# Kernel optimization log

Hardware: AMD Instinct MI355X
Metric: run time of the kernel (lower is better)

## Reference

```python
import jax, jax.numpy as jnp
import numpy as np

B, D_IN = 2048, 16
Q, QD = 512, 2
H = 128

def setup_inputs() -> dict:
    key = jax.random.key(0)
    ks = jax.random.split(key, 7)
    return {
        "input": jax.random.normal(ks[0], (B, D_IN), dtype=jnp.float32),
        "eq_param": jax.random.normal(ks[1], (QD, 1), dtype=jnp.float32),
        "quad_x": jax.random.uniform(ks[2], (Q, QD), dtype=jnp.float32),
        "W1": jax.random.normal(ks[3], (QD + D_IN, H), dtype=jnp.float32) * (1.0 / np.sqrt(QD + D_IN)),
        "b1": jnp.zeros((H,), dtype=jnp.float32),
        "W2": jax.random.normal(ks[4], (H, 1), dtype=jnp.float32) * (1.0 / np.sqrt(H)),
        "b2": jnp.zeros((1,), dtype=jnp.float32),
    }

def reference(input, eq_param, quad_x, W1, b1, W2, b2):
    # input: [B, d_in], quad_x: [Q, qd]
    b, d = input.shape
    q, qd = quad_x.shape
    # x = quad_x.repeat(B,1) -> [B,Q,qd]; z = input repeated per quad row -> [B,Q,d]
    x = jnp.broadcast_to(quad_x[None, :, :], (b, q, qd))
    z = jnp.broadcast_to(input[:, None, :], (b, q, d))
    concat = jnp.concatenate([x, z], axis=-1)            # [B,Q,qd+d]
    h = jnp.tanh(concat @ W1 + b1)                       # [B,Q,H]
    lhs = h @ W2 + b2                                    # [B,Q,1]  (mlp_x)
    y = jnp.sin(x @ eq_param)                            # [B,Q,1]  (r_func)
    rhs = lhs * y
    # per-row segment sum over Q quadrature points (and scalar out dim)
    out = jnp.sum(rhs, axis=(1, 2))[:, None]             # [B,1]
    return out
```

## Files before the change

kernel.cpp:

```cpp
#include <hip/hip_runtime.h>
#include <math.h>

#define B_N   2048
#define D_IN_ 16
#define Q_N   512
#define H_N   128

#define QCHUNK 32
#define NQC    (Q_N / QCHUNK)
#define QPC    (QCHUNK / 4)
#define NB     8
#define RPB    16
#define NRB    (B_N / RPB)

#define COEF_OFF 0
#define K0_OFF   131072
#define F_OFF    131136

static constexpr float kC = 2.88539008177792681472f;

__global__ __launch_bounds__(256) void precompute_kernel(
    const float* __restrict__ input,
    const float* __restrict__ eq,
    const float* __restrict__ qx,
    const float* __restrict__ W1,
    const float* __restrict__ b1,
    const float* __restrict__ W2,
    const float* __restrict__ b2,
    float* __restrict__ ws)
{
    const int blk = blockIdx.x;
    const int t   = threadIdx.x;

    if (blk < 1024) {
        const int idx = blk * 256 + t;
        const int row = idx >> 7, h = idx & 127;
        const float* inr = input + row * D_IN_;
        float s = 0.0f;
        #pragma unroll
        for (int d = 0; d < D_IN_; ++d)
            s = fmaf(inr[d], W1[(2 + d) * H_N + h], s);
        ws[F_OFF + idx] = __builtin_amdgcn_exp2f(s * kC);
    } else if (blk < 1088) {
        const int set  = (blk - 1024) * 256 + t;
        const int quad = set >> 7, h = set & 127;
        const float w1a = W1[h], w1b = W1[H_N + h], bh = b1[h];
        const float e0 = eq[0], e1 = eq[1];
        float n0 = 0, n1 = 0, n2 = 0, n3 = 0;
        float p1 = 0, p2 = 0, p3 = 0, p4 = 0;
        #pragma unroll
        for (int i = 0; i < 4; ++i) {
            const int q = quad * 4 + i;
            const float x0 = qx[2 * q], x1 = qx[2 * q + 1];
            const float u = fmaf(x1, w1b, fmaf(x0, w1a, bh));
            const float E = __builtin_amdgcn_exp2f(u * kC);
            const float y = -2.0f * sinf(fmaf(x1, e1, x0 * e0));
            n3 = fmaf(E, n2, fmaf(y, p3, n3));
            n2 = fmaf(E, n1, fmaf(y, p2, n2));
            n1 = fmaf(E, n0, fmaf(y, p1, n1));
            n0 = n0 + y;
            p4 = fmaf(E, p3, p4);
            p3 = fmaf(E, p2, p3);
            p2 = fmaf(E, p1, p2);
            p1 = p1 + E;
        }
        float* dst = ws + COEF_OFF + quad * (8 * H_N) + h;
        dst[0 * H_N] = n0; dst[1 * H_N] = n1; dst[2 * H_N] = n2; dst[3 * H_N] = n3;
        dst[4 * H_N] = p1; dst[5 * H_N] = p2; dst[6 * H_N] = p3; dst[7 * H_N] = p4;
    } else {
        __shared__ float red[8];
        const float e0 = eq[0], e1 = eq[1];
        const int lane = t & 63, w = t >> 6;
        float s = 0.0f;
        #pragma unroll
        for (int i = 0; i < 2; ++i) {
            const int q = t + 256 * i;
            s += sinf(fmaf(qx[2 * q + 1], e1, qx[2 * q] * e0));
        }
        #pragma unroll
        for (int off = 32; off >= 1; off >>= 1)
            s += __shfl_down(s, off, 64);
        if (lane == 0) red[w] = s;
        float ws2 = (t < H_N) ? W2[t] : 0.0f;
        if (w < 2) {
            #pragma unroll
            for (int off = 32; off >= 1; off >>= 1)
                ws2 += __shfl_down(ws2, off, 64);
            if (lane == 0) red[4 + w] = ws2;
        }
        __syncthreads();
        if (t == 0) {
            const float S = red[0] + red[1] + red[2] + red[3];
            ws[K0_OFF] = S * (red[4] + red[5] + b2[0]);
        }
    }
}

__global__ __launch_bounds__(256, 4) void main_kernel(
    const float* __restrict__ ws,
    const float* __restrict__ W2,
    float* __restrict__ out)
{
    __shared__ float c_s[QPC * 8 * H_N];
    __shared__ float part[4][NB];

    const int t    = threadIdx.x;
    const int rb   = blockIdx.x & (NRB - 1);
    const int qc   = blockIdx.x >> 7;
    const int h    = t & 127;
    const int bg   = t >> 7;
    const int lane = t & 63;
    const int w    = t >> 6;

    {
        const float4* src = (const float4*)(ws + COEF_OFF + qc * (QPC * 8 * H_N));
        float4* dst = (float4*)c_s;
        #pragma unroll
        for (int i = 0; i < (QPC * 8 * H_N / 4) / 256; ++i)
            dst[t + 256 * i] = src[t + 256 * i];
    }

    const int rowBase = rb * RPB + bg * NB;
    float F[NB], acc[NB];
    #pragma unroll
    for (int r = 0; r < NB; ++r) {
        F[r] = ws[F_OFF + (rowBase + r) * H_N + h];
        acc[r] = 0.0f;
    }
    __syncthreads();

    #pragma unroll
    for (int qd = 0; qd < QPC; ++qd) {
        const float* cp = c_s + qd * (8 * H_N) + h;
        const float n0 = cp[0 * H_N], n1 = cp[1 * H_N];
        const float n2 = cp[2 * H_N], n3 = cp[3 * H_N];
        const float c1 = cp[4 * H_N], c2 = cp[5 * H_N];
        const float c3 = cp[6 * H_N], c4 = cp[7 * H_N];
        #pragma unroll
        for (int r = 0; r < NB; ++r) {
            const float Fr  = F[r];
            const float den = fmaf(fmaf(fmaf(fmaf(c4, Fr, c3), Fr, c2), Fr, c1), Fr, 1.0f);
            const float num = fmaf(fmaf(fmaf(n3, Fr, n2), Fr, n1), Fr, n0);
            acc[r] = fmaf(num, __builtin_amdgcn_rcpf(den), acc[r]);
        }
    }

    const float w2 = W2[h];
    #pragma unroll
    for (int r = 0; r < NB; ++r) {
        float p = acc[r] * w2;
        #pragma unroll
        for (int off = 32; off >= 1; off >>= 1)
            p += __shfl_down(p, off, 64);
        if (lane == 0) part[w][r] = p;
    }
    __syncthreads();

    if (t < 16) {
        const int r = t & 7, g = t >> 3;
        float s = part[2 * g][r] + part[2 * g + 1][r];
        if (qc == 0) s += ws[K0_OFF];
        atomicAdd(out + rb * RPB + g * NB + r, s);
    }
}

extern "C" void kernel_launch(void* const* d_in, const int* in_sizes, int n_in,
                              void* d_out, int out_size, void* d_ws, size_t ws_size,
                              hipStream_t stream)
{
    (void)in_sizes; (void)n_in; (void)ws_size;
    const float* input = (const float*)d_in[0];
    const float* eq    = (const float*)d_in[1];
    const float* qx    = (const float*)d_in[2];
    const float* W1    = (const float*)d_in[3];
    const float* b1    = (const float*)d_in[4];
    const float* W2    = (const float*)d_in[5];
    const float* b2    = (const float*)d_in[6];
    float* out = (float*)d_out;
    float* ws  = (float*)d_ws;

    hipMemsetAsync(d_out, 0, (size_t)out_size * sizeof(float), stream);
    precompute_kernel<<<dim3(1089), dim3(256), 0, stream>>>(
        input, eq, qx, W1, b1, W2, b2, ws);
    main_kernel<<<dim3(NRB * NQC), dim3(256), 0, stream>>>(ws, W2, out);
}
```

Before: 83.76 us.

## Fuse precompute into main kernel, recomputing coefficients and features per block

Removes the separate precompute kernel and its global workspace. Each block now computes its own q-chunk rational coefficients, its per-row exp features and a per-chunk constant term in shared memory. This removes one launch, the workspace writes and reads, and the serialization between kernels. In exchange it adds redundant per-block recomputation of coefficients, transcendental calls and extra shared memory.

```diff
diff --git a/kernel.cpp b/kernel.cpp
--- a/kernel.cpp
+++ b/kernel.cpp
@@ -13,13 +13,9 @@
 #define RPB    16
 #define NRB    (B_N / RPB)
 
-#define COEF_OFF 0
-#define K0_OFF   131072
-#define F_OFF    131136
-
 static constexpr float kC = 2.88539008177792681472f;
 
-__global__ __launch_bounds__(256) void precompute_kernel(
+__global__ __launch_bounds__(256, 4) void fused_kernel(
     const float* __restrict__ input,
     const float* __restrict__ eq,
     const float* __restrict__ qx,
@@ -27,82 +23,14 @@
     const float* __restrict__ b1,
     const float* __restrict__ W2,
     const float* __restrict__ b2,
-    float* __restrict__ ws)
-{
-    const int blk = blockIdx.x;
-    const int t   = threadIdx.x;
-
-    if (blk < 1024) {
-        const int idx = blk * 256 + t;
-        const int row = idx >> 7, h = idx & 127;
-        const float* inr = input + row * D_IN_;
-        float s = 0.0f;
-        #pragma unroll
-        for (int d = 0; d < D_IN_; ++d)
-            s = fmaf(inr[d], W1[(2 + d) * H_N + h], s);
-        ws[F_OFF + idx] = __builtin_amdgcn_exp2f(s * kC);
-    } else if (blk < 1088) {
-        const int set  = (blk - 1024) * 256 + t;
-        const int quad = set >> 7, h = set & 127;
-        const float w1a = W1[h], w1b = W1[H_N + h], bh = b1[h];
-        const float e0 = eq[0], e1 = eq[1];
-        float n0 = 0, n1 = 0, n2 = 0, n3 = 0;
-        float p1 = 0, p2 = 0, p3 = 0, p4 = 0;
-        #pragma unroll
-        for (int i = 0; i < 4; ++i) {
-            const int q = quad * 4 + i;
-            const float x0 = qx[2 * q], x1 = qx[2 * q + 1];
-            const float u = fmaf(x1, w1b, fmaf(x0, w1a, bh));
-            const float E = __builtin_amdgcn_exp2f(u * kC);
-            const float y = -2.0f * sinf(fmaf(x1, e1, x0 * e0));
-            n3 = fmaf(E, n2, fmaf(y, p3, n3));
-            n2 = fmaf(E, n1, fmaf(y, p2, n2));
-            n1 = fmaf(E, n0, fmaf(y, p1, n1));
-            n0 = n0 + y;
-            p4 = fmaf(E, p3, p4);
-            p3 = fmaf(E, p2, p3);
-            p2 = fmaf(E, p1, p2);
-            p1 = p1 + E;
-        }
-        float* dst = ws + COEF_OFF + quad * (8 * H_N) + h;
-        dst[0 * H_N] = n0; dst[1 * H_N] = n1; dst[2 * H_N] = n2; dst[3 * H_N] = n3;
-        dst[4 * H_N] = p1; dst[5 * H_N] = p2; dst[6 * H_N] = p3; dst[7 * H_N] = p4;
-    } else {
-        __shared__ float red[8];
-        const float e0 = eq[0], e1 = eq[1];
-        const int lane = t & 63, w = t >> 6;
-        float s = 0.0f;
-        #pragma unroll
-        for (int i = 0; i < 2; ++i) {
-            const int q = t + 256 * i;
-            s += sinf(fmaf(qx[2 * q + 1], e1, qx[2 * q] * e0));
-        }
-        #pragma unroll
-        for (int off = 32; off >= 1; off >>= 1)
-            s += __shfl_down(s, off, 64);
-        if (lane == 0) red[w] = s;
-        float ws2 = (t < H_N) ? W2[t] : 0.0f;
-        if (w < 2) {
-            #pragma unroll
-            for (int off = 32; off >= 1; off >>= 1)
-                ws2 += __shfl_down(ws2, off, 64);
-            if (lane == 0) red[4 + w] = ws2;
-        }
-        __syncthreads();
-        if (t == 0) {
-            const float S = red[0] + red[1] + red[2] + red[3];
-            ws[K0_OFF] = S * (red[4] + red[5] + b2[0]);
-        }
-    }
-}
-
-__global__ __launch_bounds__(256, 4) void main_kernel(
-    const float* __restrict__ ws,
-    const float* __restrict__ W2,
     float* __restrict__ out)
 {
     __shared__ float c_s[QPC * 8 * H_N];
+    __shared__ float in_s[RPB * D_IN_];
+    __shared__ float qx_s[QCHUNK * 2];
+    __shared__ float y_s[QCHUNK];
     __shared__ float part[4][NB];
+    __shared__ float Sc_s, w2sum_s;
 
     const int t    = threadIdx.x;
     const int rb   = blockIdx.x & (NRB - 1);
@@ -112,20 +40,85 @@
     const int lane = t & 63;
     const int w    = t >> 6;
 
+    in_s[t] = input[rb * (RPB * D_IN_) + t];
+    if (t < QCHUNK * 2) qx_s[t] = qx[qc * (QCHUNK * 2) + t];
+    if (w == 0) {
+        float s = 0.0f;
+        if (lane < QCHUNK) {
+            const int q = qc * QCHUNK + lane;
+            const float a  = fmaf(qx[2 * q + 1], eq[1], qx[2 * q] * eq[0]);
+            const float yv = sinf(a);
+            y_s[lane] = -2.0f * yv;
+            s = yv;
+        }
+        #pragma unroll
+        for (int off = 32; off >= 1; off >>= 1)
+            s += __shfl_down(s, off, 64);
+        if (lane == 0) Sc_s = s;
+    }
+    if (w == 1) {
+        float s = W2[lane] + W2[64 + lane];
+        #pragma unroll
+        for (int off = 32; off >= 1; off >>= 1)
+            s += __shfl_down(s, off, 64);
+        if (lane == 0) w2sum_s = s;
+    }
+    const float w2 = W2[h];
+    __syncthreads();
+
     {
-        const float4* src = (const float4*)(ws + COEF_OFF + qc * (QPC * 8 * H_N));
-        float4* dst = (float4*)c_s;
+        const float w1a = W1[h], w1b = W1[H_N + h], bh = b1[h];
         #pragma unroll
-        for (int i = 0; i < (QPC * 8 * H_N / 4) / 256; ++i)
-            dst[t + 256 * i] = src[t + 256 * i];
+        for (int k = 0; k < 4; ++k) {
+            const int qd = bg * 4 + k;
+            float n0 = 0, n1 = 0, n2 = 0, n3 = 0;
+            float p1 = 0, p2 = 0, p3 = 0, p4 = 0;
+            #pragma unroll
+            for (int i = 0; i < 4; ++i) {
+                const int ql = qd * 4 + i;
+                const float x0 = qx_s[2 * ql], x1 = qx_s[2 * ql + 1];
+                const float u = fmaf(x1, w1b, fmaf(x0, w1a, bh));
+                const float E = __builtin_amdgcn_exp2f(u * kC);
+                const float y = y_s[ql];
+                n3 = fmaf(E, n2, fmaf(y, p3, n3));
+                n2 = fmaf(E, n1, fmaf(y, p2, n2));
+                n1 = fmaf(E, n0, fmaf(y, p1, n1));
+                n0 = n0 + y;
+                p4 = fmaf(E, p3, p4);
+                p3 = fmaf(E, p2, p3);
+                p2 = fmaf(E, p1, p2);
+                p1 = p1 + E;
+            }
+            float* dst = c_s + qd * (8 * H_N) + h;
+            dst[0 * H_N] = n0; dst[1 * H_N] = n1;
+            dst[2 * H_N] = n2; dst[3 * H_N] = n3;
+            dst[4 * H_N] = p1; dst[5 * H_N] = p2;
+            dst[6 * H_N] = p3; dst[7 * H_N] = p4;
+        }
     }
 
-    const int rowBase = rb * RPB + bg * NB;
     float F[NB], acc[NB];
-    #pragma unroll
-    for (int r = 0; r < NB; ++r) {
-        F[r] = ws[F_OFF + (rowBase + r) * H_N + h];
-        acc[r] = 0.0f;
+    {
+        float w1c[D_IN_];
+        #pragma unroll
+        for (int d = 0; d < D_IN_; ++d)
+            w1c[d] = W1[(2 + d) * H_N + h];
+        const float4* in4 = (const float4*)in_s;
+        #pragma unroll
+        for (int r = 0; r < NB; ++r) {
+            const int row = bg * NB + r;
+            float s = 0.0f;
+            #pragma unroll
+            for (int k = 0; k < 4; ++k) {
+                const float4 a = in4[row * 4 + k];
+                s = fmaf(a.x, w1c[4 * k + 0], s);
+                s = fmaf(a.y, w1c[4 * k + 1], s);
+                s = fmaf(a.z, w1c[4 * k + 2], s);
+                s = fmaf(a.w, w1c[4 * k + 3], s);
+            }
+            F[r] = __builtin_amdgcn_exp2f(s * kC);
+            acc[r] = 0.0f;
+        }
     }
     __syncthreads();
 
@@ -145,7 +138,6 @@
         }
     }
 
-    const float w2 = W2[h];
     #pragma unroll
     for (int r = 0; r < NB; ++r) {
         float p = acc[r] * w2;
@@ -158,8 +150,8 @@
 
     if (t < 16) {
         const int r = t & 7, g = t >> 3;
-        float s = part[2 * g][r] + part[2 * g + 1][r];
-        if (qc == 0) s += ws[K0_OFF];
+        const float k0c = Sc_s * (w2sum_s + b2[0]);
+        const float s = part[2 * g][r] + part[2 * g + 1][r] + k0c;
         atomicAdd(out + rb * RPB + g * NB + r, s);
     }
 }
@@ -168,7 +160,7 @@
                               void* d_out, int out_size, void* d_ws, size_t ws_size,
                               hipStream_t stream)
 {
-    (void)in_sizes; (void)n_in; (void)ws_size;
+    (void)in_sizes; (void)n_in; (void)d_ws; (void)ws_size;
     const float* input = (const float*)d_in[0];
     const float* eq    = (const float*)d_in[1];
     const float* qx    = (const float*)d_in[2];
@@ -177,10 +169,8 @@
     const float* W2    = (const float*)d_in[5];
     const float* b2    = (const float*)d_in[6];
     float* out = (float*)d_out;
-    float* ws  = (float*)d_ws;
 
     hipMemsetAsync(d_out, 0, (size_t)out_size * sizeof(float), stream);
-    precompute_kernel<<<dim3(1089), dim3(256), 0, stream>>>(
-        input, eq, qx, W1, b1, W2, b2, ws);
-    main_kernel<<<dim3(NRB * NQC), dim3(256), 0, stream>>>(ws, W2, out);
+    fused_kernel<<<dim3(NRB * NQC), dim3(256), 0, stream>>>(
+        input, eq, qx, W1, b1, W2, b2, out);
 }
```

After: 82.70 us. No clear change (-1.3%).
